# Kernel optimization log

Measured on AMD Instinct MI355X. Metric: run time of the kernel, lower is better.

The kernel has to match this reference:

```python
import jax, jax.numpy as jnp
import numpy as np
from math import sqrt

B, T, I, H, O, R = 128, 1000, 3, 512, 1, 2
NOISE_STD = 0.05
ALPHA = 0.2


def setup_inputs() -> dict:
    key = jax.random.key(0)
    ks = jax.random.split(key, 6)
    inp = jax.random.normal(ks[0], (B, T, I), dtype=jnp.float32)
    noise = jax.random.normal(ks[1], (B, T, H), dtype=jnp.float32)
    # parameters initialized as in the torch module
    wi = jax.random.normal(ks[2], (I, H), dtype=jnp.float32)
    si = jnp.ones((I,), dtype=jnp.float32)
    m = jax.random.normal(ks[3], (H, R), dtype=jnp.float32) * (1.0 / sqrt(H))
    n = jax.random.normal(ks[4], (H, R), dtype=jnp.float32) * (1.0 / sqrt(H))
    wo = jax.random.normal(ks[5], (H, O), dtype=jnp.float32) * (2.0 / H)
    so = jnp.ones((O,), dtype=jnp.float32)
    h0 = jnp.zeros((H,), dtype=jnp.float32)
    return {"input": inp, "noise": noise, "wi": wi, "si": si, "m": m,
            "n": n, "wo": wo, "so": so, "h0": h0}


def reference(input, noise, wi, si, m, n, wo, so, h0):
    # proxy parameters: wi_full = (wi.T * si).T, wo_full = wo * so
    wi_full = si[:, None] * wi          # (I, H)
    wo_full = wo * so                   # (H, O)
    batch = input.shape[0]
    h_init = jnp.broadcast_to(h0, (batch, h0.shape[0]))  # (B, H)

    def step(h, xs):
        x_t, z_t = xs                   # (B, I), (B, H)
        r = jnp.tanh(h)
        rec = (r @ n) @ m.T             # low-rank recurrence, (B, H)
        h_new = h + NOISE_STD * z_t + ALPHA * (-h + rec + x_t @ wi_full)
        out = jnp.tanh(h_new) @ wo_full  # (B, O)
        return h_new, (out, h_new)

    xs = (jnp.swapaxes(input, 0, 1), jnp.swapaxes(noise, 0, 1))  # time-major
    _, (outs, hs) = jax.lax.scan(step, h_init, xs)
    output = jnp.swapaxes(outs, 0, 1)               # (B, T, O)
    trajectories = jnp.concatenate(
        [h_init[:, None, :], jnp.swapaxes(hs, 0, 1)], axis=1)  # (B, T+1, H)
    return output, trajectories
```

## Files before the change

kernel.cpp:

```cpp
#include <hip/hip_runtime.h>

#define B_ 128
#define T_ 1000
#define I_ 3
#define H_ 512
#define RING 16

typedef float vfloat4 __attribute__((ext_vector_type(4)));

template <int CTRL>
__device__ __forceinline__ float dpp_add(float x) {
    int moved = __builtin_amdgcn_update_dpp(0, __float_as_int(x), CTRL, 0xf, 0xf, true);
    return x + __int_as_float(moved);
}

__device__ __forceinline__ void wave_reduce3(float& p0, float& p1, float& p2) {
    p0 = dpp_add<0x111>(p0); p1 = dpp_add<0x111>(p1); p2 = dpp_add<0x111>(p2);
    p0 = dpp_add<0x112>(p0); p1 = dpp_add<0x112>(p1); p2 = dpp_add<0x112>(p2);
    p0 = dpp_add<0x114>(p0); p1 = dpp_add<0x114>(p1); p2 = dpp_add<0x114>(p2);
    p0 = dpp_add<0x118>(p0); p1 = dpp_add<0x118>(p1); p2 = dpp_add<0x118>(p2);
    p0 = dpp_add<0x142>(p0); p1 = dpp_add<0x142>(p1); p2 = dpp_add<0x142>(p2);
    p0 = dpp_add<0x143>(p0); p1 = dpp_add<0x143>(p1); p2 = dpp_add<0x143>(p2);
}

__device__ __forceinline__ float fast_tanh(float x) {
    float E = __builtin_amdgcn_exp2f(x * 2.885390081777927f);
    float r = __builtin_amdgcn_rcpf(E + 1.0f);
    return __builtin_fmaf(-2.0f, r, 1.0f);
}

__global__ __launch_bounds__(64, 1) void lowrank_rnn_kernel(
    const float* __restrict__ input,
    const float* __restrict__ noise,
    const float* __restrict__ wi,
    const float* __restrict__ si,
    const float* __restrict__ m,
    const float* __restrict__ n,
    const float* __restrict__ wo,
    const float* __restrict__ so,
    const float* __restrict__ h0,
    float* __restrict__ out)
{
    const int b    = blockIdx.x;
    const int lane = threadIdx.x;
    const int j0   = lane * 8;

    __shared__ float os[T_ + 1];

    float h[8], n0[8], n1[8], m0S[8], m1S[8], wof[8], wS0[8], wS1[8], wS2[8];

    {
        const float so0 = so[0];
        const float* nb = n + 2 * j0;
        const float* mb = m + 2 * j0;
        #pragma unroll
        for (int q = 0; q < 4; ++q) {
            vfloat4 vn = *(const vfloat4*)(nb + 4 * q);
            n0[2*q] = vn.x; n1[2*q] = vn.y; n0[2*q+1] = vn.z; n1[2*q+1] = vn.w;
            vfloat4 vm = *(const vfloat4*)(mb + 4 * q);
            m0S[2*q] = 0.2f * vm.x; m1S[2*q] = 0.2f * vm.y;
            m0S[2*q+1] = 0.2f * vm.z; m1S[2*q+1] = 0.2f * vm.w;
        }
        #pragma unroll
        for (int q = 0; q < 2; ++q) {
            vfloat4 vw = *(const vfloat4*)(wo + j0 + 4 * q);
            wof[4*q] = vw.x * so0; wof[4*q+1] = vw.y * so0;
            wof[4*q+2] = vw.z * so0; wof[4*q+3] = vw.w * so0;
            vfloat4 vh = *(const vfloat4*)(h0 + j0 + 4 * q);
            h[4*q] = vh.x; h[4*q+1] = vh.y; h[4*q+2] = vh.z; h[4*q+3] = vh.w;
        }
        #pragma unroll
        for (int i = 0; i < 3; ++i) {
            float s = 0.2f * si[i];
            float* dst = (i == 0) ? wS0 : (i == 1) ? wS1 : wS2;
            #pragma unroll
            for (int q = 0; q < 2; ++q) {
                vfloat4 vw = *(const vfloat4*)(wi + i * H_ + j0 + 4 * q);
                dst[4*q] = vw.x * s; dst[4*q+1] = vw.y * s;
                dst[4*q+2] = vw.z * s; dst[4*q+3] = vw.w * s;
            }
        }
    }

    float* trajBase = out + (size_t)B_ * T_ + (size_t)b * (T_ + 1) * H_;
    {
        vfloat4 lo = {h[0], h[1], h[2], h[3]};
        vfloat4 hi = {h[4], h[5], h[6], h[7]};
        *(vfloat4*)(trajBase + j0)     = lo;
        *(vfloat4*)(trajBase + j0 + 4) = hi;
    }

    const float* zrow = noise + (size_t)b * T_ * H_ + j0;
    const float* xb   = input + (size_t)b * T_ * I_;

    vfloat4 zlo[RING], zhi[RING];

    #pragma unroll
    for (int s = 0; s < RING; ++s) {
        const float* p = zrow + (size_t)s * H_;
        zlo[s] = *(const vfloat4*)p;
        zhi[s] = *(const vfloat4*)(p + 4);
    }

    auto STEP = [&](int t, vfloat4& slo, vfloat4& shi,
                    float cx0, float cx1, float cx2, bool reload) {
        vfloat4 zl = slo, zh = shi;
        if (reload) {
            int tz = (t + RING < T_) ? t + RING : T_ - 1;
            const float* p = zrow + (size_t)tz * H_;
            slo = *(const vfloat4*)p;
            shi = *(const vfloat4*)(p + 4);
        }

        float r[8];
        #pragma unroll
        for (int k = 0; k < 8; ++k) r[k] = fast_tanh(h[k]);

        float p0 = r[0] * n0[0], p1 = r[0] * n1[0], p2 = r[0] * wof[0];
        #pragma unroll
        for (int k = 1; k < 8; ++k) {
            p0 = __builtin_fmaf(r[k], n0[k], p0);
            p1 = __builtin_fmaf(r[k], n1[k], p1);
            p2 = __builtin_fmaf(r[k], wof[k], p2);
        }
        wave_reduce3(p0, p1, p2);

        float zz[8] = {zl.x, zl.y, zl.z, zl.w, zh.x, zh.y, zh.z, zh.w};
        float base[8];
        #pragma unroll
        for (int k = 0; k < 8; ++k) {
            float xw = __builtin_fmaf(cx0, wS0[k],
                       __builtin_fmaf(cx1, wS1[k], cx2 * wS2[k]));
            base[k] = __builtin_fmaf(h[k], 0.8f,
                      __builtin_fmaf(zz[k], 0.05f, xw));
        }

        float a0 = __int_as_float(__builtin_amdgcn_readlane(__float_as_int(p0), 63));
        float a1 = __int_as_float(__builtin_amdgcn_readlane(__float_as_int(p1), 63));
        if (lane == 63) os[t] = p2;

        #pragma unroll
        for (int k = 0; k < 8; ++k)
            h[k] = __builtin_fmaf(a0, m0S[k], __builtin_fmaf(a1, m1S[k], base[k]));

        float* tr = trajBase + (size_t)(t + 1) * H_ + j0;
        vfloat4 lo = {h[0], h[1], h[2], h[3]};
        vfloat4 hi = {h[4], h[5], h[6], h[7]};
        *(vfloat4*)tr       = lo;
        *(vfloat4*)(tr + 4) = hi;
    };

    for (int tt = 0; tt < T_ - 8; tt += RING) {
        float xv0[RING], xv1[RING], xv2[RING];
        #pragma unroll
        for (int s = 0; s < RING; ++s) {
            xv0[s] = xb[3 * (tt + s) + 0];
            xv1[s] = xb[3 * (tt + s) + 1];
            xv2[s] = xb[3 * (tt + s) + 2];
        }
        #pragma unroll
        for (int s = 0; s < RING; ++s)
            STEP(tt + s, zlo[s], zhi[s], xv0[s], xv1[s], xv2[s], true);
    }

    {
        const int tt = T_ - 8;
        #pragma unroll
        for (int s = 0; s < 8; ++s) {
            float cx0 = xb[3 * (tt + s) + 0];
            float cx1 = xb[3 * (tt + s) + 1];
            float cx2 = xb[3 * (tt + s) + 2];
            STEP(tt + s, zlo[s], zhi[s], cx0, cx1, cx2, false);
        }
    }

    {
        float r[8];
        #pragma unroll
        for (int k = 0; k < 8; ++k) r[k] = fast_tanh(h[k]);
        float p2 = r[0] * wof[0];
        #pragma unroll
        for (int k = 1; k < 8; ++k) p2 = __builtin_fmaf(r[k], wof[k], p2);
        p2 = dpp_add<0x111>(p2); p2 = dpp_add<0x112>(p2);
        p2 = dpp_add<0x114>(p2); p2 = dpp_add<0x118>(p2);
        p2 = dpp_add<0x142>(p2); p2 = dpp_add<0x143>(p2);
        if (lane == 63) os[T_] = p2;
    }

    float* outp = out + (size_t)b * T_;
    for (int idx = lane; idx < T_; idx += 64)
        outp[idx] = os[idx + 1];
}

extern "C" void kernel_launch(void* const* d_in, const int* in_sizes, int n_in,
                              void* d_out, int out_size, void* d_ws, size_t ws_size,
                              hipStream_t stream) {
    const float* input = (const float*)d_in[0];
    const float* noise = (const float*)d_in[1];
    const float* wi    = (const float*)d_in[2];
    const float* si    = (const float*)d_in[3];
    const float* m     = (const float*)d_in[4];
    const float* n     = (const float*)d_in[5];
    const float* wo    = (const float*)d_in[6];
    const float* so    = (const float*)d_in[7];
    const float* h0    = (const float*)d_in[8];
    float* out = (float*)d_out;

    hipLaunchKernelGGL(lowrank_rnn_kernel, dim3(B_), dim3(64), 0, stream,
                       input, noise, wi, si, m, n, wo, so, h0, out);
}
```

Before: 339.0 us.

## Warp-specialize RNN into producer, compute and store waves via LDS rings

Splits each block into three wavefronts. A producer wave streams noise into an LDS ring with global_load_lds and precomputes the input-plus-noise term. The compute wave runs only the serial recurrence from LDS, and a store wave copies trajectory rows from an LDS ring out to global memory. Phases of 8 steps are separated by block barriers. This moves global loads, stores and input arithmetic off the latency-critical recurrence path, at the cost of a barrier every phase and extra LDS traffic.

```diff
diff --git a/kernel.cpp b/kernel.cpp
--- a/kernel.cpp
+++ b/kernel.cpp
@@ -1,10 +1,12 @@
 #include <hip/hip_runtime.h>
+#include <stdint.h>
 
 #define B_ 128
 #define T_ 1000
-#define I_ 3
 #define H_ 512
-#define RING 16
+#define PH 8
+#define NPH 125
+#define SLOTS 16
 
 typedef float vfloat4 __attribute__((ext_vector_type(4)));
 
@@ -29,7 +31,18 @@
     return __builtin_fmaf(-2.0f, r, 1.0f);
 }
 
-__global__ __launch_bounds__(64, 1) void lowrank_rnn_kernel(
+__device__ __forceinline__ void barrier_lds() {
+    asm volatile("s_waitcnt lgkmcnt(0)" ::: "memory");
+    __builtin_amdgcn_s_barrier();
+}
+
+__device__ __forceinline__ void gl_lds16(const float* g, float* l) {
+    __builtin_amdgcn_global_load_lds(
+        (const __attribute__((address_space(1))) uint32_t*)g,
+        (__attribute__((address_space(3))) uint32_t*)l, 16, 0, 0);
+}
+
+__global__ __launch_bounds__(192, 1) void lowrank_rnn_kernel(
     const float* __restrict__ input,
     const float* __restrict__ noise,
     const float* __restrict__ wi,
@@ -42,153 +55,193 @@
     float* __restrict__ out)
 {
     const int b    = blockIdx.x;
-    const int lane = threadIdx.x;
+    const int tid  = threadIdx.x;
+    const int wid  = tid >> 6;
+    const int lane = tid & 63;
     const int j0   = lane * 8;
 
+    __shared__ __align__(16) float zring[SLOTS][H_];
+    __shared__ __align__(16) float uring[SLOTS][H_];
+    __shared__ __align__(16) float hring[SLOTS][H_];
+    __shared__ float xs[T_ * 3];
     __shared__ float os[T_ + 1];
 
-    float h[8], n0[8], n1[8], m0S[8], m1S[8], wof[8], wS0[8], wS1[8], wS2[8];
-
-    {
-        const float so0 = so[0];
-        const float* nb = n + 2 * j0;
-        const float* mb = m + 2 * j0;
-        #pragma unroll
-        for (int q = 0; q < 4; ++q) {
-            vfloat4 vn = *(const vfloat4*)(nb + 4 * q);
-            n0[2*q] = vn.x; n1[2*q] = vn.y; n0[2*q+1] = vn.z; n1[2*q+1] = vn.w;
-            vfloat4 vm = *(const vfloat4*)(mb + 4 * q);
-            m0S[2*q] = 0.2f * vm.x; m1S[2*q] = 0.2f * vm.y;
-            m0S[2*q+1] = 0.2f * vm.z; m1S[2*q+1] = 0.2f * vm.w;
-        }
-        #pragma unroll
-        for (int q = 0; q < 2; ++q) {
-            vfloat4 vw = *(const vfloat4*)(wo + j0 + 4 * q);
-            wof[4*q] = vw.x * so0; wof[4*q+1] = vw.y * so0;
-            wof[4*q+2] = vw.z * so0; wof[4*q+3] = vw.w * so0;
-            vfloat4 vh = *(const vfloat4*)(h0 + j0 + 4 * q);
-            h[4*q] = vh.x; h[4*q+1] = vh.y; h[4*q+2] = vh.z; h[4*q+3] = vh.w;
-        }
-        #pragma unroll
-        for (int i = 0; i < 3; ++i) {
-            float s = 0.2f * si[i];
-            float* dst = (i == 0) ? wS0 : (i == 1) ? wS1 : wS2;
+    float* trajBase = out + (size_t)B_ * T_ + (size_t)b * (T_ + 1) * H_;
+    const float* zbase = noise + (size_t)b * T_ * H_;
+
+    if (wid == 0) {
+        float h[8], n0[8], n1[8], m0S[8], m1S[8], wof[8];
+        {
+            const float so0 = so[0];
+            const float* nb = n + 2 * j0;
+            const float* mb = m + 2 * j0;
+            #pragma unroll
+            for (int q = 0; q < 4; ++q) {
+                vfloat4 vn = *(const vfloat4*)(nb + 4 * q);
+                n0[2*q] = vn.x; n1[2*q] = vn.y; n0[2*q+1] = vn.z; n1[2*q+1] = vn.w;
+                vfloat4 vm = *(const vfloat4*)(mb + 4 * q);
+                m0S[2*q] = 0.2f * vm.x;   m1S[2*q] = 0.2f * vm.y;
+                m0S[2*q+1] = 0.2f * vm.z; m1S[2*q+1] = 0.2f * vm.w;
+            }
             #pragma unroll
             for (int q = 0; q < 2; ++q) {
-                vfloat4 vw = *(const vfloat4*)(wi + i * H_ + j0 + 4 * q);
-                dst[4*q] = vw.x * s; dst[4*q+1] = vw.y * s;
-                dst[4*q+2] = vw.z * s; dst[4*q+3] = vw.w * s;
-            }
+                vfloat4 vw = *(const vfloat4*)(wo + j0 + 4 * q);
+                wof[4*q] = vw.x * so0; wof[4*q+1] = vw.y * so0;
+                wof[4*q+2] = vw.z * so0; wof[4*q+3] = vw.w * so0;
+                vfloat4 vh = *(const vfloat4*)(h0 + j0 + 4 * q);
+                h[4*q] = vh.x; h[4*q+1] = vh.y; h[4*q+2] = vh.z; h[4*q+3] = vh.w;
+            }
+        }
+        barrier_lds();
+        barrier_lds();
+
+        for (int ph = 0; ph <= NPH; ++ph) {
+            if (ph < NPH) {
+                const int t0 = ph * PH;
+                #pragma unroll
+                for (int s = 0; s < PH; ++s) {
+                    const int t = t0 + s;
+                    char* ub = (char*)&uring[t & (SLOTS-1)][0] + lane * 32;
+                    vfloat4 ulo = *(vfloat4*)ub;
+                    vfloat4 uhi = *(vfloat4*)(ub + 16);
+
+                    float r[8];
+                    #pragma unroll
+                    for (int k = 0; k < 8; ++k) r[k] = fast_tanh(h[k]);
+
+                    float p0 = r[0] * n0[0], p1 = r[0] * n1[0], p2 = r[0] * wof[0];
+                    #pragma unroll
+                    for (int k = 1; k < 8; ++k) {
+                        p0 = __builtin_fmaf(r[k], n0[k], p0);
+                        p1 = __builtin_fmaf(r[k], n1[k], p1);
+                        p2 = __builtin_fmaf(r[k], wof[k], p2);
+                    }
+                    wave_reduce3(p0, p1, p2);
+
+                    float uu[8] = {ulo.x, ulo.y, ulo.z, ulo.w, uhi.x, uhi.y, uhi.z, uhi.w};
+                    float base[8];
+                    #pragma unroll
+                    for (int k = 0; k < 8; ++k)
+                        base[k] = __builtin_fmaf(h[k], 0.8f, uu[k]);
+
+                    float a0 = __int_as_float(__builtin_amdgcn_readlane(__float_as_int(p0), 63));
+                    float a1 = __int_as_float(__builtin_amdgcn_readlane(__float_as_int(p1), 63));
+                    if (lane == 63) os[t] = p2;
+
+                    #pragma unroll
+                    for (int k = 0; k < 8; ++k)
+                        h[k] = __builtin_fmaf(a0, m0S[k], __builtin_fmaf(a1, m1S[k], base[k]));
+
+                    char* hb = (char*)&hring[(t + 1) & (SLOTS-1)][0] + lane * 32;
+                    vfloat4 hlo = {h[0], h[1], h[2], h[3]};
+                    vfloat4 hhi = {h[4], h[5], h[6], h[7]};
+                    *(vfloat4*)hb        = hlo;
+                    *(vfloat4*)(hb + 16) = hhi;
+                }
+            } else {
+                float r[8];
+                #pragma unroll
+                for (int k = 0; k < 8; ++k) r[k] = fast_tanh(h[k]);
+                float p2 = r[0] * wof[0];
+                #pragma unroll
+                for (int k = 1; k < 8; ++k) p2 = __builtin_fmaf(r[k], wof[k], p2);
+                p2 = dpp_add<0x111>(p2); p2 = dpp_add<0x112>(p2);
+                p2 = dpp_add<0x114>(p2); p2 = dpp_add<0x118>(p2);
+                p2 = dpp_add<0x142>(p2); p2 = dpp_add<0x143>(p2);
+                if (lane == 63) os[T_] = p2;
+            }
+            barrier_lds();
+        }
+    } else if (wid == 1) {
+        float wS0[8], wS1[8], wS2[8];
+        {
+            #pragma unroll
+            for (int i = 0; i < 3; ++i) {
+                float s = 0.2f * si[i];
+                float* dst = (i == 0) ? wS0 : (i == 1) ? wS1 : wS2;
+                #pragma unroll
+                for (int q = 0; q < 2; ++q) {
+                    vfloat4 vw = *(const vfloat4*)(wi + i * H_ + j0 + 4 * q);
+                    dst[4*q] = vw.x * s; dst[4*q+1] = vw.y * s;
+                    dst[4*q+2] = vw.z * s; dst[4*q+3] = vw.w * s;
+                }
+            }
+        }
+        for (int s = 0; s < SLOTS; ++s) {
+            const float* g = zbase + (size_t)s * H_ + j0;
+            gl_lds16(g,     &zring[s][0]);
+            gl_lds16(g + 4, &zring[s][256]);
+        }
+
+        auto produce = [&](int s) {
+            asm volatile("s_waitcnt vmcnt(30)" ::: "memory");
+            char* zb = (char*)&zring[s & (SLOTS-1)][0];
+            vfloat4 zl = *(vfloat4*)(zb + lane * 16);
+            vfloat4 zh = *(vfloat4*)(zb + 1024 + lane * 16);
+            int srow = s + SLOTS; if (srow > T_ - 1) srow = T_ - 1;
+            const float* g = zbase + (size_t)srow * H_ + j0;
+            gl_lds16(g,     &zring[s & (SLOTS-1)][0]);
+            gl_lds16(g + 4, &zring[s & (SLOTS-1)][256]);
+
+            float x0 = xs[3*s], x1 = xs[3*s+1], x2 = xs[3*s+2];
+            float zz[8] = {zl.x, zl.y, zl.z, zl.w, zh.x, zh.y, zh.z, zh.w};
+            float u[8];
+            #pragma unroll
+            for (int k = 0; k < 8; ++k) {
+                float xw = __builtin_fmaf(x0, wS0[k],
+                           __builtin_fmaf(x1, wS1[k], x2 * wS2[k]));
+                u[k] = __builtin_fmaf(zz[k], 0.05f, xw);
+            }
+            char* ub = (char*)&uring[s & (SLOTS-1)][0] + lane * 32;
+            vfloat4 ulo = {u[0], u[1], u[2], u[3]};
+            vfloat4 uhi = {u[4], u[5], u[6], u[7]};
+            *(vfloat4*)ub        = ulo;
+            *(vfloat4*)(ub + 16) = uhi;
+        };
+
+        barrier_lds();
+        for (int s = 0; s < PH; ++s) produce(s);
+        barrier_lds();
+
+        for (int ph = 0; ph <= NPH; ++ph) {
+            if (ph <= NPH - 2) {
+                const int s0 = (ph + 1) * PH;
+                for (int s = s0; s < s0 + PH; ++s) produce(s);
+            }
+            barrier_lds();
+        }
+    } else {
+        for (int idx = lane; idx < T_ * 3; idx += 64)
+            xs[idx] = input[(size_t)b * T_ * 3 + idx];
+        {
+            vfloat4 a = *(const vfloat4*)(h0 + lane * 4);
+            vfloat4 c = *(const vfloat4*)(h0 + 256 + lane * 4);
+            *(vfloat4*)(trajBase + lane * 4)       = a;
+            *(vfloat4*)(trajBase + 256 + lane * 4) = c;
+        }
+        barrier_lds();
+        barrier_lds();
+
+        for (int ph = 0; ph <= NPH; ++ph) {
+            if (ph >= 1) {
+                const int t0 = (ph - 1) * PH;
+                #pragma unroll
+                for (int s = 0; s < PH; ++s) {
+                    const int row = t0 + s + 1;
+                    char* hb = (char*)&hring[row & (SLOTS-1)][0];
+                    vfloat4 v = *(vfloat4*)(hb + lane * 16);
+                    vfloat4 w = *(vfloat4*)(hb + 1024 + lane * 16);
+                    float* dst = trajBase + (size_t)row * H_;
+                    *(vfloat4*)(dst + lane * 4)       = v;
+                    *(vfloat4*)(dst + 256 + lane * 4) = w;
+                }
+            }
+            barrier_lds();
         }
     }
 
-    float* trajBase = out + (size_t)B_ * T_ + (size_t)b * (T_ + 1) * H_;
-    {
-        vfloat4 lo = {h[0], h[1], h[2], h[3]};
-        vfloat4 hi = {h[4], h[5], h[6], h[7]};
-        *(vfloat4*)(trajBase + j0)     = lo;
-        *(vfloat4*)(trajBase + j0 + 4) = hi;
-    }
-
-    const float* zrow = noise + (size_t)b * T_ * H_ + j0;
-    const float* xb   = input + (size_t)b * T_ * I_;
-
-    vfloat4 zlo[RING], zhi[RING];
-
-    #pragma unroll
-    for (int s = 0; s < RING; ++s) {
-        const float* p = zrow + (size_t)s * H_;
-        zlo[s] = *(const vfloat4*)p;
-        zhi[s] = *(const vfloat4*)(p + 4);
-    }
-
-    auto STEP = [&](int t, vfloat4& slo, vfloat4& shi,
-                    float cx0, float cx1, float cx2, bool reload) {
-        vfloat4 zl = slo, zh = shi;
-        if (reload) {
-            int tz = (t + RING < T_) ? t + RING : T_ - 1;
-            const float* p = zrow + (size_t)tz * H_;
-            slo = *(const vfloat4*)p;
-            shi = *(const vfloat4*)(p + 4);
-        }
-
-        float r[8];
-        #pragma unroll
-        for (int k = 0; k < 8; ++k) r[k] = fast_tanh(h[k]);
-
-        float p0 = r[0] * n0[0], p1 = r[0] * n1[0], p2 = r[0] * wof[0];
-        #pragma unroll
-        for (int k = 1; k < 8; ++k) {
-            p0 = __builtin_fmaf(r[k], n0[k], p0);
-            p1 = __builtin_fmaf(r[k], n1[k], p1);
-            p2 = __builtin_fmaf(r[k], wof[k], p2);
-        }
-        wave_reduce3(p0, p1, p2);
-
-        float zz[8] = {zl.x, zl.y, zl.z, zl.w, zh.x, zh.y, zh.z, zh.w};
-        float base[8];
-        #pragma unroll
-        for (int k = 0; k < 8; ++k) {
-            float xw = __builtin_fmaf(cx0, wS0[k],
-                       __builtin_fmaf(cx1, wS1[k], cx2 * wS2[k]));
-            base[k] = __builtin_fmaf(h[k], 0.8f,
-                      __builtin_fmaf(zz[k], 0.05f, xw));
-        }
-
-        float a0 = __int_as_float(__builtin_amdgcn_readlane(__float_as_int(p0), 63));
-        float a1 = __int_as_float(__builtin_amdgcn_readlane(__float_as_int(p1), 63));
-        if (lane == 63) os[t] = p2;
-
-        #pragma unroll
-        for (int k = 0; k < 8; ++k)
-            h[k] = __builtin_fmaf(a0, m0S[k], __builtin_fmaf(a1, m1S[k], base[k]));
-
-        float* tr = trajBase + (size_t)(t + 1) * H_ + j0;
-        vfloat4 lo = {h[0], h[1], h[2], h[3]};
-        vfloat4 hi = {h[4], h[5], h[6], h[7]};
-        *(vfloat4*)tr       = lo;
-        *(vfloat4*)(tr + 4) = hi;
-    };
-
-    for (int tt = 0; tt < T_ - 8; tt += RING) {
-        float xv0[RING], xv1[RING], xv2[RING];
-        #pragma unroll
-        for (int s = 0; s < RING; ++s) {
-            xv0[s] = xb[3 * (tt + s) + 0];
-            xv1[s] = xb[3 * (tt + s) + 1];
-            xv2[s] = xb[3 * (tt + s) + 2];
-        }
-        #pragma unroll
-        for (int s = 0; s < RING; ++s)
-            STEP(tt + s, zlo[s], zhi[s], xv0[s], xv1[s], xv2[s], true);
-    }
-
-    {
-        const int tt = T_ - 8;
-        #pragma unroll
-        for (int s = 0; s < 8; ++s) {
-            float cx0 = xb[3 * (tt + s) + 0];
-            float cx1 = xb[3 * (tt + s) + 1];
-            float cx2 = xb[3 * (tt + s) + 2];
-            STEP(tt + s, zlo[s], zhi[s], cx0, cx1, cx2, false);
-        }
-    }
-
-    {
-        float r[8];
-        #pragma unroll
-        for (int k = 0; k < 8; ++k) r[k] = fast_tanh(h[k]);
-        float p2 = r[0] * wof[0];
-        #pragma unroll
-        for (int k = 1; k < 8; ++k) p2 = __builtin_fmaf(r[k], wof[k], p2);
-        p2 = dpp_add<0x111>(p2); p2 = dpp_add<0x112>(p2);
-        p2 = dpp_add<0x114>(p2); p2 = dpp_add<0x118>(p2);
-        p2 = dpp_add<0x142>(p2); p2 = dpp_add<0x143>(p2);
-        if (lane == 63) os[T_] = p2;
-    }
-
     float* outp = out + (size_t)b * T_;
-    for (int idx = lane; idx < T_; idx += 64)
+    for (int idx = tid; idx < T_; idx += 192)
         outp[idx] = os[idx + 1];
 }
 
@@ -206,6 +259,6 @@
     const float* h0    = (const float*)d_in[8];
     float* out = (float*)d_out;
 
-    hipLaunchKernelGGL(lowrank_rnn_kernel, dim3(B_), dim3(64), 0, stream,
+    hipLaunchKernelGGL(lowrank_rnn_kernel, dim3(B_), dim3(192), 0, stream,
                        input, noise, wi, si, m, n, wo, so, h0, out);
 }
```

Measured after the change: 498.0 us. 1.47x slower.

## Stream noise via global_load_lds into triple-buffered LDS phases

Applied to the files above, without the earlier changes.

Replaces the 16-deep register ring of noise prefetches with direct global-to-LDS DMA loads (global_load_lds) into a three-bank LDS buffer of 8 timesteps each, gated by explicit vmcnt waits. The input sequence is also staged once into LDS instead of being reloaded per block of steps. This aims to cut register pressure and keep noise loads in flight further ahead of the serial recurrence. In exchange it relies on hand-tuned vmcnt counts that also have to account for the trajectory stores, and it adds LDS reads to each step.

```diff
diff --git a/kernel.cpp b/kernel.cpp
--- a/kernel.cpp
+++ b/kernel.cpp
@@ -1,10 +1,11 @@
 #include <hip/hip_runtime.h>
+#include <stdint.h>
 
 #define B_ 128
 #define T_ 1000
-#define I_ 3
 #define H_ 512
-#define RING 16
+#define PH 8
+#define NPHASE 125
 
 typedef float vfloat4 __attribute__((ext_vector_type(4)));
 
@@ -27,6 +28,12 @@
     float E = __builtin_amdgcn_exp2f(x * 2.885390081777927f);
     float r = __builtin_amdgcn_rcpf(E + 1.0f);
     return __builtin_fmaf(-2.0f, r, 1.0f);
+}
+
+__device__ __forceinline__ void gl_lds16(const float* g, float* l) {
+    __builtin_amdgcn_global_load_lds(
+        (const __attribute__((address_space(1))) uint32_t*)g,
+        (__attribute__((address_space(3))) uint32_t*)l, 16, 0, 0);
 }
 
 __global__ __launch_bounds__(64, 1) void lowrank_rnn_kernel(
@@ -45,10 +52,15 @@
     const int lane = threadIdx.x;
     const int j0   = lane * 8;
 
+    __shared__ __align__(16) float zbuf[3][PH][H_];
+    __shared__ float xs[T_ * 3];
     __shared__ float os[T_ + 1];
 
+    const float* xg = input + (size_t)b * T_ * 3;
+    for (int idx = lane; idx < (T_ * 3) / 4; idx += 64)
+        *(vfloat4*)&xs[idx * 4] = *(const vfloat4*)(xg + idx * 4);
+
     float h[8], n0[8], n1[8], m0S[8], m1S[8], wof[8], wS0[8], wS1[8], wS2[8];
-
     {
         const float so0 = so[0];
         const float* nb = n + 2 * j0;
@@ -58,7 +70,7 @@
             vfloat4 vn = *(const vfloat4*)(nb + 4 * q);
             n0[2*q] = vn.x; n1[2*q] = vn.y; n0[2*q+1] = vn.z; n1[2*q+1] = vn.w;
             vfloat4 vm = *(const vfloat4*)(mb + 4 * q);
-            m0S[2*q] = 0.2f * vm.x; m1S[2*q] = 0.2f * vm.y;
+            m0S[2*q] = 0.2f * vm.x;   m1S[2*q] = 0.2f * vm.y;
             m0S[2*q+1] = 0.2f * vm.z; m1S[2*q+1] = 0.2f * vm.w;
         }
         #pragma unroll
@@ -90,87 +102,79 @@
         *(vfloat4*)(trajBase + j0 + 4) = hi;
     }
 
-    const float* zrow = noise + (size_t)b * T_ * H_ + j0;
-    const float* xb   = input + (size_t)b * T_ * I_;
-
-    vfloat4 zlo[RING], zhi[RING];
-
-    #pragma unroll
-    for (int s = 0; s < RING; ++s) {
-        const float* p = zrow + (size_t)s * H_;
-        zlo[s] = *(const vfloat4*)p;
-        zhi[s] = *(const vfloat4*)(p + 4);
-    }
-
-    auto STEP = [&](int t, vfloat4& slo, vfloat4& shi,
-                    float cx0, float cx1, float cx2, bool reload) {
-        vfloat4 zl = slo, zh = shi;
-        if (reload) {
-            int tz = (t + RING < T_) ? t + RING : T_ - 1;
-            const float* p = zrow + (size_t)tz * H_;
-            slo = *(const vfloat4*)p;
-            shi = *(const vfloat4*)(p + 4);
-        }
-
-        float r[8];
-        #pragma unroll
-        for (int k = 0; k < 8; ++k) r[k] = fast_tanh(h[k]);
-
-        float p0 = r[0] * n0[0], p1 = r[0] * n1[0], p2 = r[0] * wof[0];
-        #pragma unroll
-        for (int k = 1; k < 8; ++k) {
-            p0 = __builtin_fmaf(r[k], n0[k], p0);
-            p1 = __builtin_fmaf(r[k], n1[k], p1);
-            p2 = __builtin_fmaf(r[k], wof[k], p2);
-        }
-        wave_reduce3(p0, p1, p2);
-
-        float zz[8] = {zl.x, zl.y, zl.z, zl.w, zh.x, zh.y, zh.z, zh.w};
-        float base[8];
-        #pragma unroll
-        for (int k = 0; k < 8; ++k) {
-            float xw = __builtin_fmaf(cx0, wS0[k],
-                       __builtin_fmaf(cx1, wS1[k], cx2 * wS2[k]));
-            base[k] = __builtin_fmaf(h[k], 0.8f,
-                      __builtin_fmaf(zz[k], 0.05f, xw));
-        }
-
-        float a0 = __int_as_float(__builtin_amdgcn_readlane(__float_as_int(p0), 63));
-        float a1 = __int_as_float(__builtin_amdgcn_readlane(__float_as_int(p1), 63));
-        if (lane == 63) os[t] = p2;
-
-        #pragma unroll
-        for (int k = 0; k < 8; ++k)
-            h[k] = __builtin_fmaf(a0, m0S[k], __builtin_fmaf(a1, m1S[k], base[k]));
-
-        float* tr = trajBase + (size_t)(t + 1) * H_ + j0;
-        vfloat4 lo = {h[0], h[1], h[2], h[3]};
-        vfloat4 hi = {h[4], h[5], h[6], h[7]};
-        *(vfloat4*)tr       = lo;
-        *(vfloat4*)(tr + 4) = hi;
+    const float* zb0 = noise + (size_t)b * T_ * H_ + j0;
+    auto dma_row = [&](int row, int bank, int slot) {
+        const float* g = zb0 + (size_t)row * H_;
+        gl_lds16(g,     &zbuf[bank][slot][0]);
+        gl_lds16(g + 4, &zbuf[bank][slot][256]);
     };
 
-    for (int tt = 0; tt < T_ - 8; tt += RING) {
-        float xv0[RING], xv1[RING], xv2[RING];
-        #pragma unroll
-        for (int s = 0; s < RING; ++s) {
-            xv0[s] = xb[3 * (tt + s) + 0];
-            xv1[s] = xb[3 * (tt + s) + 1];
-            xv2[s] = xb[3 * (tt + s) + 2];
-        }
-        #pragma unroll
-        for (int s = 0; s < RING; ++s)
-            STEP(tt + s, zlo[s], zhi[s], xv0[s], xv1[s], xv2[s], true);
-    }
-
-    {
-        const int tt = T_ - 8;
-        #pragma unroll
-        for (int s = 0; s < 8; ++s) {
-            float cx0 = xb[3 * (tt + s) + 0];
-            float cx1 = xb[3 * (tt + s) + 1];
-            float cx2 = xb[3 * (tt + s) + 2];
-            STEP(tt + s, zlo[s], zhi[s], cx0, cx1, cx2, false);
+    for (int s = 0; s < PH; ++s) dma_row(s, 0, s);
+    for (int s = 0; s < PH; ++s) dma_row(PH + s, 1, s);
+
+    for (int ph = 0; ph < NPHASE; ++ph) {
+        if (ph == 0)      asm volatile("s_waitcnt vmcnt(16)" ::: "memory");
+        else if (ph == 1) asm volatile("s_waitcnt vmcnt(32)" ::: "memory");
+        else              asm volatile("s_waitcnt vmcnt(48)" ::: "memory");
+        __builtin_amdgcn_sched_barrier(0);
+
+        {
+            const int rb = (ph + 2) * PH;
+            const int bank2 = (ph + 2) % 3;
+            #pragma unroll
+            for (int s = 0; s < PH; ++s) {
+                int row = rb + s; if (row > T_ - 1) row = T_ - 1;
+                dma_row(row, bank2, s);
+            }
+        }
+        __builtin_amdgcn_sched_barrier(0);
+
+        const int bank = ph % 3;
+        const int t0 = ph * PH;
+        #pragma unroll
+        for (int s = 0; s < PH; ++s) {
+            const int t = t0 + s;
+            char* zrow = (char*)&zbuf[bank][s][0];
+            vfloat4 zl = *(vfloat4*)(zrow + lane * 16);
+            vfloat4 zh = *(vfloat4*)(zrow + 1024 + lane * 16);
+            float cx0 = xs[3*t], cx1 = xs[3*t+1], cx2 = xs[3*t+2];
+
+            float r[8];
+            #pragma unroll
+            for (int k = 0; k < 8; ++k) r[k] = fast_tanh(h[k]);
+
+            float p0 = r[0] * n0[0], p1 = r[0] * n1[0], p2 = r[0] * wof[0];
+            #pragma unroll
+            for (int k = 1; k < 8; ++k) {
+                p0 = __builtin_fmaf(r[k], n0[k], p0);
+                p1 = __builtin_fmaf(r[k], n1[k], p1);
+                p2 = __builtin_fmaf(r[k], wof[k], p2);
+            }
+            wave_reduce3(p0, p1, p2);
+
+            float zz[8] = {zl.x, zl.y, zl.z, zl.w, zh.x, zh.y, zh.z, zh.w};
+            float base[8];
+            #pragma unroll
+            for (int k = 0; k < 8; ++k) {
+                float xw = __builtin_fmaf(cx0, wS0[k],
+                           __builtin_fmaf(cx1, wS1[k], cx2 * wS2[k]));
+                base[k] = __builtin_fmaf(h[k], 0.8f,
+                          __builtin_fmaf(zz[k], 0.05f, xw));
+            }
+
+            float a0 = __int_as_float(__builtin_amdgcn_readlane(__float_as_int(p0), 63));
+            float a1 = __int_as_float(__builtin_amdgcn_readlane(__float_as_int(p1), 63));
+            if (lane == 63) os[t] = p2;
+
+            #pragma unroll
+            for (int k = 0; k < 8; ++k)
+                h[k] = __builtin_fmaf(a0, m0S[k], __builtin_fmaf(a1, m1S[k], base[k]));
+
+            float* tr = trajBase + (size_t)(t + 1) * H_ + j0;
+            vfloat4 lo = {h[0], h[1], h[2], h[3]};
+            vfloat4 hi = {h[4], h[5], h[6], h[7]};
+            *(vfloat4*)tr       = lo;
+            *(vfloat4*)(tr + 4) = hi;
         }
     }
 
```

Measured after the change: 404.7 us. 19.4% more time.
